# Optimization experiments

Hardware: AMD Instinct MI355X
Metric: run time of the kernel (lower is better)

Reference implementation:

```python
import jax, jax.numpy as jnp
import numpy as np
from jax import lax

Z, Y, X = 9, 5, 5          # anchor grid (AnchorInit)
A = Z * Y * X              # 225 anchors
NS = 8                     # nsample in AnchorGrouping
H = 64                     # feature / hidden width


def anchor_template():
    # (Z,Y,X,3) grid of anchor coordinates, last dim ordered (x,y,z) so that
    # anchors[:,:,:2] += g_loc shifts the planar (x,y) location.
    xs = (jnp.arange(X, dtype=jnp.float32) - (X - 1) / 2.0) * 0.2
    ys = (jnp.arange(Y, dtype=jnp.float32) - (Y - 1) / 2.0) * 0.2
    zs = jnp.arange(Z, dtype=jnp.float32) * 0.22 + 0.1
    gz, gy, gx = jnp.meshgrid(zs, ys, xs, indexing='ij')
    return jnp.stack([gx, gy, gz], axis=-1)


def setup_inputs() -> dict:
    key = jax.random.key(0)
    ks = jax.random.split(key, 16)
    B, T, N, F = 16, 64, 128, 2
    M = B * T
    s = 0.1
    f32 = jnp.float32
    return {
        'x': jax.random.normal(ks[0], (M, N, 3 + F), f32),
        'g_loc': jax.random.normal(ks[1], (B, T, 2), f32) * 0.5,
        'h0': jnp.zeros((1, B, H), f32),
        'c0': jnp.zeros((1, B, H), f32),
        # AnchorPointNet: per-point MLP 5->16->32->64 + attention pooling
        'pn_w1': jax.random.normal(ks[2], (3 + F, 16), f32) * s,
        'pn_b1': jnp.zeros((16,), f32),
        'pn_w2': jax.random.normal(ks[3], (16, 32), f32) * s,
        'pn_b2': jnp.zeros((32,), f32),
        'pn_w3': jax.random.normal(ks[4], (32, H), f32) * s,
        'pn_b3': jnp.zeros((H,), f32),
        'attn_w': jax.random.normal(ks[5], (H, 1), f32) * s,
        'attn_b': jnp.zeros((1,), f32),
        # AnchorVoxelNet: Conv3d 64->96 (3,3,3), 96->128 (3,3,3), 128->64 (5,1,1), OIDHW
        'vx_w1': jax.random.normal(ks[6], (96, 64, 3, 3, 3), f32) * s,
        'vx_b1': jnp.zeros((96,), f32),
        'vx_w2': jax.random.normal(ks[7], (128, 96, 3, 3, 3), f32) * s,
        'vx_b2': jnp.zeros((128,), f32),
        'vx_w3': jax.random.normal(ks[8], (64, 128, 5, 1, 1), f32) * s,
        'vx_b3': jnp.zeros((64,), f32),
        # AnchorRNN: 1-layer LSTM, input 64, hidden 64, torch gate order (i,f,g,o)
        'lstm_wi': jax.random.normal(ks[9], (H, 4 * H), f32) * s,
        'lstm_wh': jax.random.normal(ks[10], (H, 4 * H), f32) * s,
        'lstm_b': jnp.zeros((4 * H,), f32),
        'batch_size': 16,
        'length_size': 64,
        'feature_size': 2,
    }


def reference(x, g_loc, h0, c0,
              pn_w1, pn_b1, pn_w2, pn_b2, pn_w3, pn_b3, attn_w, attn_b,
              vx_w1, vx_b1, vx_w2, vx_b2, vx_w3, vx_b3,
              lstm_wi, lstm_wh, lstm_b,
              batch_size, length_size, feature_size):
    M = batch_size * length_size
    # ---- anchors: template grid translated by per-frame global (x,y) location
    anchors = jnp.tile(anchor_template().reshape(1, A, 3), (M, 1, 1))
    anchors = anchors.at[:, :, :2].add(g_loc.reshape(M, 1, 2))
    # ---- AnchorGrouping: 8-NN of each anchor in the radar point cloud
    xyz = x[..., :3]                      # (M,N,3)
    points = x[..., 3:]                   # (M,N,F)
    d = (jnp.sum(anchors * anchors, -1)[:, :, None]
         - 2.0 * jnp.einsum('mad,mnd->man', anchors, xyz)
         + jnp.sum(xyz * xyz, -1)[:, None, :])      # (M,A,N) squared dists
    _, idx = lax.top_k(-d, NS)                       # (M,A,8) nearest points
    bi = jnp.arange(M)[:, None, None]
    g_xyz = xyz[bi, idx] - anchors[:, :, None, :]    # (M,A,8,3) anchor-relative
    g_pts = points[bi, idx]                          # (M,A,8,F)
    grouped = jnp.concatenate([g_xyz, g_pts], -1).reshape(M * A, NS, 3 + feature_size)
    # ---- AnchorPointNet: shared MLP + attention pooling over the 8 neighbors
    f = jax.nn.relu(grouped @ pn_w1 + pn_b1)
    f = jax.nn.relu(f @ pn_w2 + pn_b2)
    f = jax.nn.relu(f @ pn_w3 + pn_b3)               # (MA,8,64)
    attn = jax.nn.softmax(f @ attn_w + attn_b, axis=1)   # (MA,8,1)
    voxel_points = jnp.sum(attn * f, axis=1)         # (MA,64)
    attn_weights = attn[..., 0]                      # (MA,8)
    # ---- AnchorVoxelNet: 3D conv over the (Z,Y,X) anchor grid
    v = voxel_points.reshape(M, Z, Y, X, H).transpose(0, 4, 1, 2, 3)  # (M,64,9,5,5)
    dn = ('NCDHW', 'OIDHW', 'NCDHW')
    v = jax.nn.relu(lax.conv_general_dilated(v, vx_w1, (1, 1, 1), 'VALID', dimension_numbers=dn)
                    + vx_b1[None, :, None, None, None])               # (M,96,7,3,3)
    v = jax.nn.relu(lax.conv_general_dilated(v, vx_w2, (1, 1, 1), 'VALID', dimension_numbers=dn)
                    + vx_b2[None, :, None, None, None])               # (M,128,5,1,1)
    v = lax.conv_general_dilated(v, vx_w3, (1, 1, 1), 'VALID', dimension_numbers=dn) \
        + vx_b3[None, :, None, None, None]                            # (M,64,1,1,1)
    voxel_vec = v.reshape(batch_size, length_size, H)
    # ---- AnchorRNN: single-layer LSTM over time
    def step(carry, xt):
        h, c = carry
        gates = xt @ lstm_wi + h @ lstm_wh + lstm_b
        i, fg, g, o = jnp.split(gates, 4, axis=-1)
        c = jax.nn.sigmoid(fg) * c + jax.nn.sigmoid(i) * jnp.tanh(g)
        h = jax.nn.sigmoid(o) * jnp.tanh(c)
        return (h, c), h
    (hn, cn), ys = lax.scan(step, (h0[0], c0[0]), voxel_vec.transpose(1, 0, 2))
    a_vec = ys.transpose(1, 0, 2)                    # (B,T,64)
    return a_vec, attn_weights, hn[None], cn[None]
```

## Files before the change

### kernel.cpp

```cpp
#include <hip/hip_runtime.h>
#include <cmath>

#define AT 225
#define NP 128
#define MT 1024
#define NSEL 8
#define HD 64

#define SZ_VOX  (1024u*64u*225u)
#define SZ_C1   (1024u*96u*63u)
#define SZ_C2   (1024u*128u*5u)
#define SZ_VV   (1024u*64u)
#define SZ_XWI  (1024u*256u)
#define SZ_W1T  (64u*27u*96u)
#define SZ_W2T  (96u*27u*128u)
#define SZ_W3T  (640u*64u)
#define SZ_W2M  (512u)

#define C2S 98

typedef __attribute__((ext_vector_type(8))) short bf16x8;
typedef __attribute__((ext_vector_type(4))) float f32x4;

__device__ __forceinline__ float sigm(float x) { return 1.0f / (1.0f + expf(-x)); }

__device__ __forceinline__ unsigned short f2bf(float f) {
    unsigned u = __float_as_uint(f);
    unsigned r = u + 0x7FFF + ((u >> 16) & 1);
    return (unsigned short)(r >> 16);
}

#if defined(__has_builtin)
#if __has_builtin(__builtin_amdgcn_cvt_pk_bf16_f32)
#define HAVE_CVT_PK_BF16 1
#endif
#endif

__device__ __forceinline__ unsigned pk2(float a, float b) {
#ifdef HAVE_CVT_PK_BF16
    auto v = __builtin_amdgcn_cvt_pk_bf16_f32(a, b);
    return __builtin_bit_cast(unsigned, v);
#else
    return (unsigned)f2bf(a) | ((unsigned)f2bf(b) << 16);
#endif
}

__global__ __launch_bounds__(256) void k_transpose(
    const float* __restrict__ w1, const float* __restrict__ w2,
    const float* __restrict__ w3, const float* __restrict__ pnw3,
    const float* __restrict__ pnw2,
    unsigned short* __restrict__ w1m, unsigned short* __restrict__ w2n,
    float* __restrict__ w3t, unsigned short* __restrict__ w3m,
    unsigned short* __restrict__ w2m)
{
    int idx = blockIdx.x * 256 + threadIdx.x;
    if (idx < 20736) {
        int lane = idx & 63, r = idx >> 6;
        int t = r % 6, s = r / 6;
        int o = t * 16 + (lane & 15);
        int kb = s * 32 + (lane >> 4) * 8;
        unsigned int dw[4];
        #pragma unroll
        for (int jd = 0; jd < 4; ++jd) {
            int k0 = kb + 2 * jd, k1 = k0 + 1;
            dw[jd] = (unsigned)f2bf(w1[o * 1728 + (k0 & 63) * 27 + (k0 >> 6)]) |
                     ((unsigned)f2bf(w1[o * 1728 + (k1 & 63) * 27 + (k1 >> 6)]) << 16);
        }
        uint4 v; v.x = dw[0]; v.y = dw[1]; v.z = dw[2]; v.w = dw[3];
        ((uint4*)w1m)[idx] = v;
    } else if (idx < 62208) {
        int q = idx - 20736;
        int lane = q & 63, r = q >> 6;
        int nt = r & 7, s = r >> 3;
        int o = nt * 16 + (lane & 15);
        int kb = s * 32 + (lane >> 4) * 8;
        unsigned int dw[4];
        #pragma unroll
        for (int jd = 0; jd < 4; ++jd) {
            int k0 = kb + 2 * jd, k1 = k0 + 1;
            dw[jd] = (unsigned)f2bf(w2[o * 2592 + (k0 % 96) * 27 + (k0 / 96)]) |
                     ((unsigned)f2bf(w2[o * 2592 + (k1 % 96) * 27 + (k1 / 96)]) << 16);
        }
        uint4 v; v.x = dw[0]; v.y = dw[1]; v.z = dw[2]; v.w = dw[3];
        ((uint4*)w2n)[q] = v;
    } else if (idx < 103168) {
        int k = idx - 62208;
        int u = k & 63, r = k >> 6;
        w3t[k] = w3[u * 640 + r];
    } else if (idx < 103424) {
        int k = idx - 103168;
        int lane = k & 63, nt = k >> 6;
        int n = nt * 16 + (lane & 15);
        int kb = (lane >> 4) * 8;
        unsigned int dw[4];
        #pragma unroll
        for (int jd = 0; jd < 4; ++jd) {
            int k0 = kb + 2 * jd;
            dw[jd] = (unsigned)f2bf(pnw3[k0 * 64 + n]) |
                     ((unsigned)f2bf(pnw3[(k0 + 1) * 64 + n]) << 16);
        }
        uint4 v; v.x = dw[0]; v.y = dw[1]; v.z = dw[2]; v.w = dw[3];
        ((uint4*)w3m)[k] = v;
    } else if (idx < 103552) {
        int k = idx - 103424;
        int lane = k & 63, nt = k >> 6;
        int n = nt * 16 + (lane & 15);
        int kb = (lane >> 4) * 8;
        unsigned int dw[4];
        #pragma unroll
        for (int jd = 0; jd < 4; ++jd) {
            int k0 = kb + 2 * jd, k1 = k0 + 1;
            float a = (k0 < 16) ? pnw2[k0 * 32 + n] : 0.0f;
            float b = (k1 < 16) ? pnw2[k1 * 32 + n] : 0.0f;
            dw[jd] = (unsigned)f2bf(a) | ((unsigned)f2bf(b) << 16);
        }
        uint4 v; v.x = dw[0]; v.y = dw[1]; v.z = dw[2]; v.w = dw[3];
        ((uint4*)w2m)[k] = v;
    }
}

__global__ __launch_bounds__(256) void k_group(
    const float* __restrict__ x, const float* __restrict__ g_loc,
    int* __restrict__ idxbuf)
{
    const int m = blockIdx.x;
    const int tid = threadIdx.x;
    __shared__ float pts[3][NP];

    for (int idx = tid; idx < NP * 5; idx += 256) {
        int n = idx / 5, c = idx % 5;
        if (c < 3) pts[c][n] = x[m * (NP * 5) + idx];
    }
    __syncthreads();

    const float gx = g_loc[m * 2 + 0], gy = g_loc[m * 2 + 1];
    const int grp = tid >> 3, li = tid & 7;

    for (int ca = 0; ca < 256; ca += 32) {
        const int a = ca + grp;
        const bool active = (a < AT);
        const int aa = active ? a : (AT - 1);
        const int azi = aa / 25, ar = aa % 25, ayi = ar / 5, axi = ar % 5;
        const float fx = ((float)axi - 2.0f) * 0.2f + gx;
        const float fy = ((float)ayi - 2.0f) * 0.2f + gy;
        const float fz = (float)azi * 0.22f + 0.1f;
        const float sa = fx * fx + fy * fy + fz * fz;

        float d[16];
        #pragma unroll
        for (int r = 0; r < 16; ++r) {
            int n = li * 16 + r;
            float px = pts[0][n], py = pts[1][n], pz = pts[2][n];
            d[r] = sa - 2.0f * (fx * px + fy * py + fz * pz)
                      + (px * px + py * py + pz * pz);
        }
        int nidx = 0;
        for (int j = 0; j < NSEL; ++j) {
            float best = 1e30f; int bidx = 0;
            #pragma unroll
            for (int r = 0; r < 16; ++r) {
                int n = li * 16 + r;
                if (d[r] < best) { best = d[r]; bidx = n; }
            }
            #pragma unroll
            for (int off = 1; off < 8; off <<= 1) {
                float ov = __shfl_xor(best, off);
                int   oi = __shfl_xor(bidx, off);
                if (ov < best || (ov == best && oi < bidx)) { best = ov; bidx = oi; }
            }
            if (li == j) nidx = bidx;
            if ((bidx >> 4) == li) {
                int slot = bidx & 15;
                #pragma unroll
                for (int r = 0; r < 16; ++r)
                    if (r == slot) d[r] = 1e30f;
            }
        }
        if (active) idxbuf[(m * AT + a) * NSEL + li] = nidx;
    }
}

__global__ __launch_bounds__(128) void k_mlpm(
    const float* __restrict__ x, const float* __restrict__ g_loc,
    const int* __restrict__ idxbuf,
    const float* __restrict__ w1, const float* __restrict__ b1,
    const unsigned short* __restrict__ w2m, const float* __restrict__ b2,
    const unsigned short* __restrict__ w3m, const float* __restrict__ b3,
    const float* __restrict__ aw, const float* __restrict__ ab,
    unsigned short* __restrict__ vox, float* __restrict__ attn_out)
{
    const int tid = threadIdx.x;
    const int row0 = blockIdx.x * 128;
    const int row = row0 + tid;

    __shared__ __align__(16) char smem[25600];
    unsigned int*   fbuf = (unsigned int*)smem;
    unsigned int*   f3w  = (unsigned int*)(smem + 8704);
    float*          pts  = (float*)(smem + 8704);
    float*          sbuf = (float*)smem;

    const int m0 = row0 / 1800;
    const int m1 = (row0 + 127) / 1800;
    #pragma unroll
    for (int i = tid; i < 640; i += 128) {
        pts[i]       = x[m0 * 640 + i];
        pts[640 + i] = x[m1 * 640 + i];
    }
    __syncthreads();

    const int m = row / 1800;
    const int rr = row % 1800;
    const int a = rr >> 3;
    const int base = (m == m0) ? 0 : 640;

    const int azi = a / 25, ar = a % 25, ayi = ar / 5, axi = ar % 5;
    const float gx = g_loc[m * 2 + 0], gy = g_loc[m * 2 + 1];
    const float fx = ((float)axi - 2.0f) * 0.2f + gx;
    const float fy = ((float)ayi - 2.0f) * 0.2f + gy;
    const float fz = (float)azi * 0.22f + 0.1f;

    const int nidx = idxbuf[row];
    const float in0 = pts[base + nidx * 5 + 0] - fx;
    const float in1 = pts[base + nidx * 5 + 1] - fy;
    const float in2 = pts[base + nidx * 5 + 2] - fz;
    const float in3 = pts[base + nidx * 5 + 3];
    const float in4 = pts[base + nidx * 5 + 4];

    float f1v[16];
    #pragma unroll
    for (int j = 0; j < 16; ++j) {
        float s = b1[j];
        s += in0 * w1[0 * 16 + j] + in1 * w1[1 * 16 + j] + in2 * w1[2 * 16 + j]
           + in3 * w1[3 * 16 + j] + in4 * w1[4 * 16 + j];
        f1v[j] = fmaxf(s, 0.0f);
    }
    __syncthreads();
    #pragma unroll
    for (int kd = 0; kd < 8; ++kd)
        fbuf[tid * 17 + kd] = pk2(f1v[2 * kd], f1v[2 * kd + 1]);
    #pragma unroll
    for (int kd = 8; kd < 16; ++kd)
        fbuf[tid * 17 + kd] = 0u;

    const int wv = tid >> 6, lane = tid & 63;
    const int quad = lane >> 4, mcol = lane & 15;

    bf16x8 w2f[2];
    #pragma unroll
    for (int nt = 0; nt < 2; ++nt) {
        uint4 u = ((const uint4*)w2m)[nt * 64 + lane];
        w2f[nt] = __builtin_bit_cast(bf16x8, u);
    }
    const float4* b24 = (const float4*)b2;
    float4 b2q[2];
    #pragma unroll
    for (int nt = 0; nt < 2; ++nt) b2q[nt] = b24[nt * 4 + quad];

    #pragma unroll
    for (int mt = 0; mt < 4; ++mt) {
        const int rowbase = (wv * 4 + mt) * 16;
        const int abase = (rowbase + mcol) * 17 + quad * 4;
        uint4 au;
        au.x = fbuf[abase + 0]; au.y = fbuf[abase + 1];
        au.z = fbuf[abase + 2]; au.w = fbuf[abase + 3];
        bf16x8 af = __builtin_bit_cast(bf16x8, au);
        #pragma unroll
        for (int nt = 0; nt < 2; ++nt) {
            f32x4 z = (f32x4){0.f, 0.f, 0.f, 0.f};
            f32x4 acc = __builtin_amdgcn_mfma_f32_16x16x32_bf16(w2f[nt], af, z, 0, 0, 0);
            float v0 = fmaxf(acc[0] + b2q[nt].x, 0.0f);
            float v1 = fmaxf(acc[1] + b2q[nt].y, 0.0f);
            float v2 = fmaxf(acc[2] + b2q[nt].z, 0.0f);
            float v3 = fmaxf(acc[3] + b2q[nt].w, 0.0f);
            const int dbase = (rowbase + mcol) * 17 + nt * 8 + quad * 2;
            fbuf[dbase + 0] = pk2(v0, v1);
            fbuf[dbase + 1] = pk2(v2, v3);
        }
    }

    bf16x8 w3f[4];
    #pragma unroll
    for (int nt = 0; nt < 4; ++nt) {
        uint4 u = ((const uint4*)w3m)[nt * 64 + lane];
        w3f[nt] = __builtin_bit_cast(bf16x8, u);
    }
    const float4* b34 = (const float4*)b3;
    float4 b3q[4];
    #pragma unroll
    for (int nt = 0; nt < 4; ++nt) b3q[nt] = b34[nt * 4 + quad];

    #pragma unroll
    for (int mt = 0; mt < 4; ++mt) {
        const int rowbase = (wv * 4 + mt) * 16;
        const int abase = (rowbase + mcol) * 17 + quad * 4;
        uint4 au;
        au.x = fbuf[abase + 0]; au.y = fbuf[abase + 1];
        au.z = fbuf[abase + 2]; au.w = fbuf[abase + 3];
        bf16x8 af = __builtin_bit_cast(bf16x8, au);
        #pragma unroll
        for (int nt = 0; nt < 4; ++nt) {
            f32x4 z = (f32x4){0.f, 0.f, 0.f, 0.f};
            f32x4 acc = __builtin_amdgcn_mfma_f32_16x16x32_bf16(w3f[nt], af, z, 0, 0, 0);
            float v0 = fmaxf(acc[0] + b3q[nt].x, 0.0f);
            float v1 = fmaxf(acc[1] + b3q[nt].y, 0.0f);
            float v2 = fmaxf(acc[2] + b3q[nt].z, 0.0f);
            float v3 = fmaxf(acc[3] + b3q[nt].w, 0.0f);
            const int dbase = (rowbase + mcol) * 33 + nt * 8 + quad * 2;
            f3w[dbase + 0] = pk2(v0, v1);
            f3w[dbase + 1] = pk2(v2, v3);
        }
    }

    const unsigned int* f3dw = (const unsigned int*)f3w;
    float s0 = 0.f, s1 = 0.f;
    #pragma unroll
    for (int kd = 0; kd < 32; ++kd) {
        unsigned dw = f3dw[tid * 33 + kd];
        s0 = fmaf(__uint_as_float(dw << 16), aw[2 * kd], s0);
        s1 = fmaf(__uint_as_float(dw & 0xFFFF0000u), aw[2 * kd + 1], s1);
    }
    float sc = s0 + s1 + ab[0];

    float mx = sc;
    #pragma unroll
    for (int off = 1; off < 8; off <<= 1) mx = fmaxf(mx, __shfl_xor(mx, off));
    float e = expf(sc - mx);
    float den = e;
    #pragma unroll
    for (int off = 1; off < 8; off <<= 1) den += __shfl_xor(den, off);
    const float at = e / den;
    attn_out[row] = at;

    const int lgrp = tid >> 3;
    const int li = tid & 7;
    const int wl = tid & 63;
    float oo[8];
    #pragma unroll
    for (int i = 0; i < 8; ++i) oo[i] = 0.0f;
    #pragma unroll
    for (int ns = 0; ns < 8; ++ns) {
        float atn = __shfl(at, (wl >> 3) * 8 + ns);
        const int rbase = (lgrp * 8 + ns) * 33;
        #pragma unroll
        for (int q = 0; q < 4; ++q) {
            unsigned dw = f3dw[rbase + q * 8 + li];
            oo[2 * q + 0] = fmaf(atn, __uint_as_float(dw << 16), oo[2 * q + 0]);
            oo[2 * q + 1] = fmaf(atn, __uint_as_float(dw & 0xFFFF0000u), oo[2 * q + 1]);
        }
    }
    __syncthreads();
    #pragma unroll
    for (int q = 0; q < 4; ++q) {
        sbuf[lgrp * 65 + q * 16 + li * 2 + 0] = oo[2 * q + 0];
        sbuf[lgrp * 65 + q * 16 + li * 2 + 1] = oo[2 * q + 1];
    }
    __syncthreads();

    const int al = tid & 15, j = tid >> 4;
    const int ga = (row0 >> 3) + al;
    const int ma = ga / 225, aa2 = ga % 225;
    #pragma unroll
    for (int rep = 0; rep < 8; ++rep) {
        int h = j * 8 + rep;
        vox[(ma * 64 + h) * AT + aa2] = f2bf(sbuf[al * 65 + h]);
    }
}

__global__ __launch_bounds__(256) void k_conv1m(
    const unsigned short* __restrict__ vox, const unsigned short* __restrict__ w1m,
    const float* __restrict__ b1, unsigned short* __restrict__ out)
{
    const int m0 = blockIdx.x * 2;
    const int tid = threadIdx.x;
    __shared__ unsigned short voxT[2][225 * 66];

    #pragma unroll
    for (int img = 0; img < 2; ++img) {
        const unsigned int* vsrc =
            (const unsigned int*)(vox + (size_t)(m0 + img) * 14400);
        for (int i = tid; i < 7200; i += 256) {
            unsigned v = vsrc[i];
            int e0 = 2 * i, e1 = e0 + 1;
            int c0 = e0 / 225, a0 = e0 - c0 * 225;
            int c1i = e1 / 225, a1 = e1 - c1i * 225;
            voxT[img][a0 * 66 + c0] = (unsigned short)(v & 0xFFFFu);
            voxT[img][a1 * 66 + c1i] = (unsigned short)(v >> 16);
        }
    }
    __syncthreads();

    const int wv = tid >> 6, lane = tid & 63;
    const int quad = lane >> 4, n = lane & 15;
    const int p = wv * 16 + n;
    const int pe = (p > 62) ? 62 : p;
    const int zo = pe / 9, pr = pe % 9, yo = pr / 3, xo = pr % 3;
    const int basep = zo * 25 + yo * 5 + xo;

    f32x4 acc[2][6];
    #pragma unroll
    for (int g = 0; g < 2; ++g)
        #pragma unroll
        for (int t = 0; t < 6; ++t) acc[g][t] = (f32x4){0.f, 0.f, 0.f, 0.f};

    const uint4* Aptr = (const uint4*)w1m;

    auto loadB = [&](int img, int s) -> uint4 {
        int tap = s >> 1;
        int dz = tap / 9, tr = tap % 9, dy = tr / 3, dx = tr % 3;
        int rw = basep + dz * 25 + dy * 5 + dx;
        int bidx = rw * 66 + (s & 1) * 32 + quad * 8;
        const unsigned int* vp = (const unsigned int*)(&voxT[img][0] + bidx);
        uint4 r; r.x = vp[0]; r.y = vp[1]; r.z = vp[2]; r.w = vp[3];
        return r;
    };

    uint4 Acur[6], Anxt[6];
    uint4 Bcur[2], Bnxt[2];
    #pragma unroll
    for (int t = 0; t < 6; ++t) Acur[t] = Aptr[t * 64 + lane];
    Bcur[0] = loadB(0, 0); Bcur[1] = loadB(1, 0);

    for (int s = 0; s < 54; ++s) {
        if ((s & 3) == 0) __syncthreads();
        if (s < 53) {
            Bnxt[0] = loadB(0, s + 1);
            Bnxt[1] = loadB(1, s + 1);
            #pragma unroll
            for (int t = 0; t < 6; ++t)
                Anxt[t] = Aptr[((s + 1) * 6 + t) * 64 + lane];
        }
        bf16x8 bf0 = __builtin_bit_cast(bf16x8, Bcur[0]);
        bf16x8 bf1 = __builtin_bit_cast(bf16x8, Bcur[1]);
        #pragma unroll
        for (int t = 0; t < 6; ++t) {
            bf16x8 af = __builtin_bit_cast(bf16x8, Acur[t]);
            acc[0][t] = __builtin_amdgcn_mfma_f32_16x16x32_bf16(af, bf0, acc[0][t], 0, 0, 0);
            acc[1][t] = __builtin_amdgcn_mfma_f32_16x16x32_bf16(af, bf1, acc[1][t], 0, 0, 0);
        }
        #pragma unroll
        for (int t = 0; t < 6; ++t) Acur[t] = Anxt[t];
        Bcur[0] = Bnxt[0]; Bcur[1] = Bnxt[1];
    }

    if (p < 63) {
        #pragma unroll
        for (int g = 0; g < 2; ++g) {
            #pragma unroll
            for (int t = 0; t < 6; ++t) {
                #pragma unroll
                for (int r = 0; r < 4; ++r) {
                    int o = t * 16 + quad * 4 + r;
                    out[(m0 + g) * (96 * 63) + o * 63 + p] =
                        f2bf(fmaxf(acc[g][t][r] + b1[o], 0.0f));
                }
            }
        }
    }
}

__global__ __launch_bounds__(256) void k_c23(
    const unsigned short* __restrict__ c1, const unsigned short* __restrict__ w2n,
    const float* __restrict__ b2, const float* __restrict__ w3t,
    const float* __restrict__ b3, const float* __restrict__ wi,
    const float* __restrict__ lb, float* __restrict__ xwi)
{
    const int tid = threadIdx.x;
    const int m0 = blockIdx.x * 2;
    __shared__ unsigned short c1T[2 * 63 * C2S];
    __shared__ float c2l[2][640];
    __shared__ float part[2][4][64];
    __shared__ float vvl[2][64];

    const unsigned int* csrc = (const unsigned int*)(c1 + (size_t)m0 * 6048);
    for (int i = tid; i < 6048; i += 256) {
        unsigned v = csrc[i];
        int e0 = 2 * i;
        int mi = (i >= 3024);
        int r0 = e0 - mi * 6048, r1 = r0 + 1;
        int o0 = r0 / 63, p0 = r0 - o0 * 63;
        int o1 = r1 / 63, p1 = r1 - o1 * 63;
        c1T[(mi * 63 + p0) * C2S + o0] = (unsigned short)(v & 0xFFFFu);
        c1T[(mi * 63 + p1) * C2S + o1] = (unsigned short)(v >> 16);
    }
    __syncthreads();

    const int wv = tid >> 6, lane = tid & 63;
    const int quad = lane >> 4, ncol = lane & 15;
    const int arow = lane & 15;
    const int mi = (arow < 10) ? arow / 5 : 1;
    const int zo = (arow < 10) ? arow % 5 : 4;

    f32x4 acc[2];
    acc[0] = (f32x4){0.f, 0.f, 0.f, 0.f};
    acc[1] = (f32x4){0.f, 0.f, 0.f, 0.f};
    const uint4* Bptr = (const uint4*)w2n;

    for (int tap = 0; tap < 27; ++tap) {
        const int dz = tap / 9, r9 = tap % 9;
        const int rowb = (mi * 63 + (zo + dz) * 9 + r9) * C2S;
        #pragma unroll
        for (int sub = 0; sub < 3; ++sub) {
            const int s = tap * 3 + sub;
            const unsigned int* ap =
                (const unsigned int*)(c1T + rowb + sub * 32 + quad * 8);
            uint4 au; au.x = ap[0]; au.y = ap[1]; au.z = ap[2]; au.w = ap[3];
            bf16x8 af = __builtin_bit_cast(bf16x8, au);
            #pragma unroll
            for (int nt = 0; nt < 2; ++nt) {
                uint4 bu = Bptr[(s * 8 + wv * 2 + nt) * 64 + lane];
                bf16x8 bf = __builtin_bit_cast(bf16x8, bu);
                acc[nt] = __builtin_amdgcn_mfma_f32_16x16x32_bf16(af, bf, acc[nt], 0, 0, 0);
            }
        }
    }

    #pragma unroll
    for (int nt = 0; nt < 2; ++nt) {
        const int o = (wv * 2 + nt) * 16 + ncol;
        const float bias = b2[o];
        #pragma unroll
        for (int reg = 0; reg < 4; ++reg) {
            int rr = quad * 4 + reg;
            if (rr < 10)
                c2l[rr / 5][o * 5 + (rr % 5)] = fmaxf(acc[nt][reg] + bias, 0.0f);
        }
    }
    __syncthreads();

    {
        const int u = tid & 63, kq = tid >> 6;
        const int k0 = kq * 160;
        #pragma unroll
        for (int mi2 = 0; mi2 < 2; ++mi2) {
            float acc3 = 0.0f;
            #pragma unroll 8
            for (int k = k0; k < k0 + 160; ++k)
                acc3 = fmaf(c2l[mi2][k], w3t[k * 64 + u], acc3);
            part[mi2][kq][u] = acc3;
        }
    }
    __syncthreads();
    if (tid < 128) {
        int mi2 = tid >> 6, u = tid & 63;
        vvl[mi2][u] = b3[u] + ((part[mi2][0][u] + part[mi2][1][u])
                    + (part[mi2][2][u] + part[mi2][3][u]));
    }
    __syncthreads();

    #pragma unroll
    for (int mi2 = 0; mi2 < 2; ++mi2) {
        float a2 = lb[tid];
        #pragma unroll
        for (int k = 0; k < 64; ++k)
            a2 = fmaf(vvl[mi2][k], wi[k * 256 + tid], a2);
        xwi[(m0 + mi2) * 256 + tid] = a2;
    }
}

__global__ __launch_bounds__(256) void k_lstm(
    const float* __restrict__ xwi, const float* __restrict__ whg,
    const float* __restrict__ h0, const float* __restrict__ c0,
    float* __restrict__ avec, float* __restrict__ hn, float* __restrict__ cn)
{
    const int b = blockIdx.x;
    const int j = threadIdx.x;
    __shared__ __align__(16) float hbuf[64];
    __shared__ float gbuf[256];

    float wh[64];
    #pragma unroll
    for (int k = 0; k < 64; ++k) wh[k] = whg[k * 256 + j];

    if (j < 64) hbuf[j] = h0[b * 64 + j];
    float c = (j < 64) ? c0[b * 64 + j] : 0.0f;
    const bool is_tanh_gate = ((j >> 6) == 2);
    __syncthreads();

    const float4* hb4 = (const float4*)hbuf;
    float xt = xwi[(b * 64 + 0) * 256 + j];
    for (int t = 0; t < 64; ++t) {
        float xt_next = (t < 63) ? xwi[(b * 64 + t + 1) * 256 + j] : 0.0f;
        float g = xt;
        float p[4] = {0.f, 0.f, 0.f, 0.f};
        #pragma unroll
        for (int k4 = 0; k4 < 16; ++k4) {
            float4 h4 = hb4[k4];
            int q = k4 & 3;
            p[q] = fmaf(h4.x, wh[4 * k4 + 0], p[q]);
            p[q] = fmaf(h4.y, wh[4 * k4 + 1], p[q]);
            p[q] = fmaf(h4.z, wh[4 * k4 + 2], p[q]);
            p[q] = fmaf(h4.w, wh[4 * k4 + 3], p[q]);
        }
        g += (p[0] + p[1]) + (p[2] + p[3]);
        gbuf[j] = is_tanh_gate ? tanhf(g) : sigm(g);
        __syncthreads();
        if (j < 64) {
            c = gbuf[64 + j] * c + gbuf[j] * gbuf[128 + j];
            float h = gbuf[192 + j] * tanhf(c);
            hbuf[j] = h;
            avec[(b * 64 + t) * 64 + j] = h;
        }
        __syncthreads();
        xt = xt_next;
    }
    if (j < 64) {
        hn[b * 64 + j] = hbuf[j];
        cn[b * 64 + j] = c;
    }
}

extern "C" void kernel_launch(void* const* d_in, const int* in_sizes, int n_in,
                              void* d_out, int out_size, void* d_ws, size_t ws_size,
                              hipStream_t stream) {
    const float* x     = (const float*)d_in[0];
    const float* g_loc = (const float*)d_in[1];
    const float* h0    = (const float*)d_in[2];
    const float* c0    = (const float*)d_in[3];
    const float* pn_w1 = (const float*)d_in[4];
    const float* pn_b1 = (const float*)d_in[5];
    const float* pn_w2 = (const float*)d_in[6];
    const float* pn_b2 = (const float*)d_in[7];
    const float* pn_w3 = (const float*)d_in[8];
    const float* pn_b3 = (const float*)d_in[9];
    const float* aw    = (const float*)d_in[10];
    const float* ab    = (const float*)d_in[11];
    const float* vx_w1 = (const float*)d_in[12];
    const float* vx_b1 = (const float*)d_in[13];
    const float* vx_w2 = (const float*)d_in[14];
    const float* vx_b2 = (const float*)d_in[15];
    const float* vx_w3 = (const float*)d_in[16];
    const float* vx_b3 = (const float*)d_in[17];
    const float* lwi   = (const float*)d_in[18];
    const float* lwh   = (const float*)d_in[19];
    const float* lb    = (const float*)d_in[20];

    float* ws  = (float*)d_ws;
    float* voxr = ws;
    float* c1r  = voxr + SZ_VOX;
    float* c2  = c1r + SZ_C1;
    float* vv  = c2 + SZ_C2;
    float* xwi = vv + SZ_VV;
    float* w1r = xwi + SZ_XWI;
    float* w2r = w1r + SZ_W1T;
    float* w3t = w2r + SZ_W2T;
    float* w2mr = w3t + SZ_W3T;
    unsigned short* voxh = (unsigned short*)voxr;
    unsigned short* c1h  = (unsigned short*)c1r;
    unsigned short* w1m = (unsigned short*)w1r;
    unsigned short* w2n = (unsigned short*)w2r;
    unsigned short* w2m = (unsigned short*)w2mr;
    unsigned short* w3m = (unsigned short*)xwi;
    int*   idxb = (int*)c1r;

    float* out   = (float*)d_out;
    float* avec  = out;
    float* attnw = out + 65536;
    float* hn    = out + 65536 + 1843200;
    float* cn    = hn + 1024;

    k_transpose<<<405, 256, 0, stream>>>(vx_w1, vx_w2, vx_w3, pn_w3, pn_w2,
                                         w1m, w2n, w3t, w3m, w2m);
    k_group<<<1024, 256, 0, stream>>>(x, g_loc, idxb);
    k_mlpm<<<14400, 128, 0, stream>>>(x, g_loc, idxb, pn_w1, pn_b1, w2m, pn_b2,
                                      w3m, pn_b3, aw, ab, voxh, attnw);
    k_conv1m<<<512, 256, 0, stream>>>(voxh, w1m, vx_b1, c1h);
    k_c23<<<512, 256, 0, stream>>>(c1h, w2n, vx_b2, w3t, vx_b3, lwi, lb, xwi);
    k_lstm<<<16, 256, 0, stream>>>(xwi, lwh, h0, c0, avec, hn, cn);
}
```

Measured before the change: 353.2 us.

## Keep MLP layer-3 outputs in registers and fuse attention pooling via shuffles

The third MLP layer's MFMA results no longer go to a padded shared-memory buffer. The attention score, the softmax over each 8-sample group and the weighted pooling are now computed directly from the accumulator registers using cross-lane shuffles, and a select tree picks each lane's output columns. This cuts shared memory from 25.6KB to 8.7KB and removes a round of LDS traffic, which allows more resident blocks; a launch-bounds minimum of 4 blocks is added to match. In exchange it adds many shuffle instructions and more register pressure.

```diff
diff --git a/kernel.cpp b/kernel.cpp
--- a/kernel.cpp
+++ b/kernel.cpp
@@ -180,7 +180,7 @@
     }
 }
 
-__global__ __launch_bounds__(128) void k_mlpm(
+__global__ __launch_bounds__(128, 4) void k_mlpm(
     const float* __restrict__ x, const float* __restrict__ g_loc,
     const int* __restrict__ idxbuf,
     const float* __restrict__ w1, const float* __restrict__ b1,
@@ -193,10 +193,9 @@
     const int row0 = blockIdx.x * 128;
     const int row = row0 + tid;
 
-    __shared__ __align__(16) char smem[25600];
+    __shared__ __align__(16) char smem[8704];
     unsigned int*   fbuf = (unsigned int*)smem;
-    unsigned int*   f3w  = (unsigned int*)(smem + 8704);
-    float*          pts  = (float*)(smem + 8704);
+    float*          pts  = (float*)smem;
     float*          sbuf = (float*)smem;
 
     const int m0 = row0 / 1800;
@@ -244,6 +243,8 @@
 
     const int wv = tid >> 6, lane = tid & 63;
     const int quad = lane >> 4, mcol = lane & 15;
+    const int hf = mcol >> 3;
+    const int j3 = mcol & 7;
 
     bf16x8 w2f[2];
     #pragma unroll
@@ -289,6 +290,16 @@
     #pragma unroll
     for (int nt = 0; nt < 4; ++nt) b3q[nt] = b34[nt * 4 + quad];
 
+    float awv[16];
+    #pragma unroll
+    for (int nt = 0; nt < 4; ++nt)
+        #pragma unroll
+        for (int rg = 0; rg < 4; ++rg)
+            awv[nt * 4 + rg] = aw[nt * 16 + quad * 4 + rg];
+    const float abv = ab[0];
+
+    float osb[8];
+
     #pragma unroll
     for (int mt = 0; mt < 4; ++mt) {
         const int rowbase = (wv * 4 + mt) * 16;
@@ -297,6 +308,8 @@
         au.x = fbuf[abase + 0]; au.y = fbuf[abase + 1];
         au.z = fbuf[abase + 2]; au.w = fbuf[abase + 3];
         bf16x8 af = __builtin_bit_cast(bf16x8, au);
+
+        float vbf[16];
         #pragma unroll
         for (int nt = 0; nt < 4; ++nt) {
             f32x4 z = (f32x4){0.f, 0.f, 0.f, 0.f};
@@ -305,54 +318,67 @@
             float v1 = fmaxf(acc[1] + b3q[nt].y, 0.0f);
             float v2 = fmaxf(acc[2] + b3q[nt].z, 0.0f);
             float v3 = fmaxf(acc[3] + b3q[nt].w, 0.0f);
-            const int dbase = (rowbase + mcol) * 33 + nt * 8 + quad * 2;
-            f3w[dbase + 0] = pk2(v0, v1);
-            f3w[dbase + 1] = pk2(v2, v3);
-        }
-    }
-
-    const unsigned int* f3dw = (const unsigned int*)f3w;
-    float s0 = 0.f, s1 = 0.f;
-    #pragma unroll
-    for (int kd = 0; kd < 32; ++kd) {
-        unsigned dw = f3dw[tid * 33 + kd];
-        s0 = fmaf(__uint_as_float(dw << 16), aw[2 * kd], s0);
-        s1 = fmaf(__uint_as_float(dw & 0xFFFF0000u), aw[2 * kd + 1], s1);
-    }
-    float sc = s0 + s1 + ab[0];
-
-    float mx = sc;
-    #pragma unroll
-    for (int off = 1; off < 8; off <<= 1) mx = fmaxf(mx, __shfl_xor(mx, off));
-    float e = expf(sc - mx);
-    float den = e;
-    #pragma unroll
-    for (int off = 1; off < 8; off <<= 1) den += __shfl_xor(den, off);
-    const float at = e / den;
-    attn_out[row] = at;
-
-    const int lgrp = tid >> 3;
-    const int li = tid & 7;
-    const int wl = tid & 63;
-    float oo[8];
-    #pragma unroll
-    for (int i = 0; i < 8; ++i) oo[i] = 0.0f;
-    #pragma unroll
-    for (int ns = 0; ns < 8; ++ns) {
-        float atn = __shfl(at, (wl >> 3) * 8 + ns);
-        const int rbase = (lgrp * 8 + ns) * 33;
-        #pragma unroll
-        for (int q = 0; q < 4; ++q) {
-            unsigned dw = f3dw[rbase + q * 8 + li];
-            oo[2 * q + 0] = fmaf(atn, __uint_as_float(dw << 16), oo[2 * q + 0]);
-            oo[2 * q + 1] = fmaf(atn, __uint_as_float(dw & 0xFFFF0000u), oo[2 * q + 1]);
-        }
-    }
-    __syncthreads();
-    #pragma unroll
-    for (int q = 0; q < 4; ++q) {
-        sbuf[lgrp * 65 + q * 16 + li * 2 + 0] = oo[2 * q + 0];
-        sbuf[lgrp * 65 + q * 16 + li * 2 + 1] = oo[2 * q + 1];
+            unsigned d0 = pk2(v0, v1), d1 = pk2(v2, v3);
+            vbf[nt * 4 + 0] = __uint_as_float(d0 << 16);
+            vbf[nt * 4 + 1] = __uint_as_float(d0 & 0xFFFF0000u);
+            vbf[nt * 4 + 2] = __uint_as_float(d1 << 16);
+            vbf[nt * 4 + 3] = __uint_as_float(d1 & 0xFFFF0000u);
+        }
+
+        float p = 0.f;
+        #pragma unroll
+        for (int c = 0; c < 16; ++c) p = fmaf(vbf[c], awv[c], p);
+        p += __shfl_xor(p, 16);
+        p += __shfl_xor(p, 32);
+        const float sc = p + abv;
+
+        float mx = sc;
+        mx = fmaxf(mx, __shfl_xor(mx, 1));
+        mx = fmaxf(mx, __shfl_xor(mx, 2));
+        mx = fmaxf(mx, __shfl_xor(mx, 4));
+        const float e = expf(sc - mx);
+        float den = e;
+        den += __shfl_xor(den, 1);
+        den += __shfl_xor(den, 2);
+        den += __shfl_xor(den, 4);
+        const float at = e / den;
+        if (quad == 0) attn_out[row0 + wv * 64 + mt * 16 + mcol] = at;
+
+        float cur[16];
+        #pragma unroll
+        for (int c = 0; c < 16; ++c) cur[c] = at * vbf[c];
+        #pragma unroll
+        for (int off = 1; off < 8; off <<= 1) {
+            #pragma unroll
+            for (int c = 0; c < 16; ++c)
+                cur[c] += __shfl_xor(cur[c], off);
+        }
+
+        float a0 = (j3 & 1) ? cur[1] : cur[0];
+        float a1 = (j3 & 1) ? cur[3] : cur[2];
+        float a2 = (j3 & 1) ? cur[5] : cur[4];
+        float a3 = (j3 & 1) ? cur[7] : cur[6];
+        float c0p = (j3 & 2) ? a1 : a0;
+        float c1p = (j3 & 2) ? a3 : a2;
+        float o0 = (j3 & 4) ? c1p : c0p;
+        float a4 = (j3 & 1) ? cur[9]  : cur[8];
+        float a5 = (j3 & 1) ? cur[11] : cur[10];
+        float a6 = (j3 & 1) ? cur[13] : cur[12];
+        float a7 = (j3 & 1) ? cur[15] : cur[14];
+        float c2p = (j3 & 2) ? a5 : a4;
+        float c3p = (j3 & 2) ? a7 : a6;
+        float o1 = (j3 & 4) ? c3p : c2p;
+        osb[2 * mt + 0] = o0;
+        osb[2 * mt + 1] = o1;
+    }
+
+    __syncthreads();
+    const int col0 = (j3 >> 2) * 16 + quad * 4 + (j3 & 3);
+    #pragma unroll
+    for (int mt = 0; mt < 4; ++mt) {
+        const int anc = wv * 8 + mt * 2 + hf;
+        sbuf[anc * 65 + col0]      = osb[2 * mt + 0];
+        sbuf[anc * 65 + col0 + 32] = osb[2 * mt + 1];
     }
     __syncthreads();
 
```

Result: slower. 403.6 us (+14.3%).
